# Optimization experiments

Hardware: AMD Instinct MI355X
Metric: run time of the kernel (lower is better)

The kernel has to match this reference:

```python
import jax, jax.numpy as jnp
import numpy as np

D_MODEL = 2048
NUM_HEADS = 32
NUM_GROUPS = 8
HEAD_DIM = D_MODEL // NUM_HEADS  # 64
HEADS_PER_GROUP = NUM_HEADS // NUM_GROUPS  # 4


def setup_inputs() -> dict:
    key = jax.random.key(0)
    ks = jax.random.split(key, 5)
    B, S = 1, 2048
    x = jax.random.normal(ks[0], (B, S, D_MODEL), dtype=jnp.float32)
    scale = 1.0 / np.sqrt(D_MODEL)
    w_q = jax.random.normal(ks[1], (D_MODEL, D_MODEL), dtype=jnp.float32) * scale
    w_k = jax.random.normal(ks[2], (D_MODEL, NUM_GROUPS * HEAD_DIM), dtype=jnp.float32) * scale
    w_v = jax.random.normal(ks[3], (D_MODEL, NUM_GROUPS * HEAD_DIM), dtype=jnp.float32) * scale
    w_o = jax.random.normal(ks[4], (D_MODEL, D_MODEL), dtype=jnp.float32) * scale
    return {"x": x, "w_q": w_q, "w_k": w_k, "w_v": w_v, "w_o": w_o}


def reference(x, w_q, w_k, w_v, w_o):
    B, S, _ = x.shape
    # projections (nn.Linear, no bias)
    q = (x @ w_q).reshape(B, S, NUM_HEADS, HEAD_DIM)          # [B,S,H,d]
    k = (x @ w_k).reshape(B, S, NUM_GROUPS, HEAD_DIM)         # [B,S,G,d]
    v = (x @ w_v).reshape(B, S, NUM_GROUPS, HEAD_DIM)
    # group queries: [B,S,G,hpg,d] so each KV group serves heads_per_group query heads
    qg = q.reshape(B, S, NUM_GROUPS, HEADS_PER_GROUP, HEAD_DIM)
    scale = 1.0 / jnp.sqrt(jnp.asarray(HEAD_DIM, dtype=x.dtype))
    # scores: [B,G,hpg,S_q,S_k] without duplicating K/V
    scores = jnp.einsum("bsghd,btgd->bghst", qg, k) * scale
    attn = jax.nn.softmax(scores, axis=-1)
    out = jnp.einsum("bghst,btgd->bsghd", attn, v)            # [B,S,G,hpg,d]
    out = out.reshape(B, S, D_MODEL)
    return out @ w_o
```

## Files before the change

### kernel.cpp

```cpp
#include <hip/hip_runtime.h>

typedef unsigned short ushort_t;
typedef __attribute__((ext_vector_type(8))) short short8;
typedef __attribute__((ext_vector_type(4))) float floatx4;

__device__ __forceinline__ unsigned short f2bf(float f) {
  unsigned int u = __float_as_uint(f);
  u += 0x7fffu + ((u >> 16) & 1u);
  return (unsigned short)(u >> 16);
}

__device__ __forceinline__ void gl_lds16(const void* g, void* l) {
  __builtin_amdgcn_global_load_lds((const __attribute__((address_space(1))) void*)g,
                                   (__attribute__((address_space(3))) void*)l,
                                   16, 0, 0);
}


__global__ void conv_x_kernel(const float* __restrict__ src, ushort_t* __restrict__ dst, int n4) {
  int i = blockIdx.x * blockDim.x + threadIdx.x;
  if (i >= n4) return;
  float4 v = ((const float4*)src)[i];
  union { ushort_t u[4]; unsigned long long ll; } o;
  o.u[0] = f2bf(v.x); o.u[1] = f2bf(v.y); o.u[2] = f2bf(v.z); o.u[3] = f2bf(v.w);
  ((unsigned long long*)dst)[i] = o.ll;
}

__global__ void transpose_conv(const float* __restrict__ src, ushort_t* __restrict__ dst,
                               int R, int C) {
  __shared__ float tile[32][33];
  int c0 = blockIdx.x * 32, r0 = blockIdx.y * 32;
  int tx = threadIdx.x, ty = threadIdx.y;
#pragma unroll
  for (int i = ty; i < 32; i += 8)
    tile[i][tx] = src[(long)(r0 + i) * C + c0 + tx];
  __syncthreads();
#pragma unroll
  for (int i = ty; i < 32; i += 8)
    dst[(long)(c0 + i) * R + r0 + tx] = f2bf(tile[tx][i]);
}

template <int EPI>
__global__ __launch_bounds__(256, 2) void gemm_bt(
    const ushort_t* __restrict__ A, const ushort_t* __restrict__ B,
    float* __restrict__ C,
    ushort_t* __restrict__ qb, ushort_t* __restrict__ kb, ushort_t* __restrict__ vb,
    int M, int N, int K) {
  __shared__ ushort_t As[128 * 32];
  __shared__ ushort_t Bs[128 * 32];
  const int t = threadIdx.x;
  const int w = t >> 6, lane = t & 63;
  const int m = lane & 15, quad = lane >> 4;
  const int m0 = blockIdx.y * 128, n0 = blockIdx.x * 128;
  const int wr = w >> 1, wc = w & 1;

  floatx4 acc[4][4] = {};

  for (int kk = 0; kk < K; kk += 32) {
    __syncthreads();
#pragma unroll
    for (int i = 0; i < 2; ++i) {
      int c = i * 256 + t;
      int c0 = i * 256 + w * 64;
      gl_lds16(A + (long)(m0 + (c >> 2)) * K + kk + (c & 3) * 8, As + c0 * 8);
      gl_lds16(B + (long)(n0 + (c >> 2)) * K + kk + (c & 3) * 8, Bs + c0 * 8);
    }
    __syncthreads();
    short8 af[4], bf[4];
#pragma unroll
    for (int i = 0; i < 4; ++i)
      af[i] = *(const short8*)(As + (wr * 64 + i * 16 + m) * 32 + quad * 8);
#pragma unroll
    for (int j = 0; j < 4; ++j)
      bf[j] = *(const short8*)(Bs + (wc * 64 + j * 16 + m) * 32 + quad * 8);
#pragma unroll
    for (int i = 0; i < 4; ++i)
#pragma unroll
      for (int j = 0; j < 4; ++j)
        acc[i][j] = __builtin_amdgcn_mfma_f32_16x16x32_bf16(af[i], bf[j], acc[i][j], 0, 0, 0);
  }

#pragma unroll
  for (int i = 0; i < 4; ++i)
#pragma unroll
    for (int j = 0; j < 4; ++j)
#pragma unroll
      for (int r = 0; r < 4; ++r) {
        float v = acc[i][j][r];
        int row = m0 + wr * 64 + i * 16 + quad * 4 + r;
        int col = n0 + wc * 64 + j * 16 + m;
        if (EPI == 1) {
          C[(long)row * N + col] = v;
        } else {
          if (col < 2048) {
            qb[((((col >> 6) * 2048) + row) << 6) | (col & 63)] = f2bf(v * 0.125f);
          } else if (col < 2560) {
            int g = (col - 2048) >> 6;
            kb[(((g * 2048) + row) << 6) | (col & 63)] = f2bf(v);
          } else {
            int g = (col - 2560) >> 6;
            vb[(long)((g << 6) | (col & 63)) * 2048 + row] = f2bf(v);
          }
        }
      }
}

__global__ __launch_bounds__(256, 2) void flash_kernel(
    const ushort_t* __restrict__ Q, const ushort_t* __restrict__ Kb,
    const ushort_t* __restrict__ Vb, ushort_t* __restrict__ O, int S) {
  __shared__ ushort_t Ks[2 * 128 * 32];
  __shared__ ushort_t Vs[4 * 64 * 32];
  __shared__ ushort_t Ps[4 * 4 * 32 * 32];
  const int t = threadIdx.x;
  const int w = t >> 6, lane = t & 63;
  const int m = lane & 15, quad = lane >> 4;
  const int h = blockIdx.y, g = h >> 2;
  const int q0 = blockIdx.x * 128;
  const ushort_t* qp = Q + (long)h * S * 64;
  const ushort_t* kp = Kb + (long)g * S * 64;
  const ushort_t* vp = Vb + (long)g * 64 * S;

  short8 qf[2][2];
#pragma unroll
  for (int rt = 0; rt < 2; ++rt)
#pragma unroll
    for (int kq = 0; kq < 2; ++kq)
      qf[rt][kq] = *(const short8*)(qp + (long)(q0 + w * 32 + rt * 16 + m) * 64 + kq * 32 + quad * 8);

  float mrow[2][4], lrow[2][4];
  floatx4 oacc[2][4] = {};
#pragma unroll
  for (int rt = 0; rt < 2; ++rt)
#pragma unroll
    for (int r = 0; r < 4; ++r) { mrow[rt][r] = -1e30f; lrow[rt][r] = 0.f; }

  ushort_t* Pw = Ps + w * 4096;

  for (int t0 = 0; t0 < S; t0 += 128) {
    __syncthreads();
#pragma unroll
    for (int i = 0; i < 4; ++i) {
      int c = i * 256 + t;
      int c0 = i * 256 + w * 64;
      gl_lds16(kp + (long)(t0 + ((c >> 2) & 127)) * 64 + (c >> 9) * 32 + (c & 3) * 8, Ks + c0 * 8);
      gl_lds16(vp + (long)((c >> 2) & 63) * S + t0 + (c >> 8) * 32 + (c & 3) * 8, Vs + c0 * 8);
    }
    __syncthreads();

    floatx4 sacc[2][8] = {};
#pragma unroll
    for (int ct = 0; ct < 8; ++ct) {
      short8 kf0 = *(const short8*)(Ks + (ct * 16 + m) * 32 + quad * 8);
      short8 kf1 = *(const short8*)(Ks + 4096 + (ct * 16 + m) * 32 + quad * 8);
#pragma unroll
      for (int rt = 0; rt < 2; ++rt) {
        sacc[rt][ct] = __builtin_amdgcn_mfma_f32_16x16x32_bf16(qf[rt][0], kf0, sacc[rt][ct], 0, 0, 0);
        sacc[rt][ct] = __builtin_amdgcn_mfma_f32_16x16x32_bf16(qf[rt][1], kf1, sacc[rt][ct], 0, 0, 0);
      }
    }

    float mnew[2][4], al[2][4], ls[2][4];
#pragma unroll
    for (int rt = 0; rt < 2; ++rt)
#pragma unroll
      for (int r = 0; r < 4; ++r) {
        float mx = sacc[rt][0][r];
#pragma unroll
        for (int ct = 1; ct < 8; ++ct) mx = fmaxf(mx, sacc[rt][ct][r]);
#pragma unroll
        for (int s = 1; s < 16; s <<= 1) mx = fmaxf(mx, __shfl_xor(mx, s));
        mnew[rt][r] = fmaxf(mrow[rt][r], mx);
        al[rt][r] = __expf(mrow[rt][r] - mnew[rt][r]);
        ls[rt][r] = 0.f;
      }

#pragma unroll
    for (int rt = 0; rt < 2; ++rt)
#pragma unroll
      for (int ct = 0; ct < 8; ++ct) {
        int kt = ct >> 1;
        int colbase = (ct & 1) * 16 + m;
#pragma unroll
        for (int r = 0; r < 4; ++r) {
          float p = __expf(sacc[rt][ct][r] - mnew[rt][r]);
          ls[rt][r] += p;
          int row = rt * 16 + quad * 4 + r;
          Pw[kt * 1024 + row * 32 + colbase] = f2bf(p);
        }
      }

#pragma unroll
    for (int rt = 0; rt < 2; ++rt)
#pragma unroll
      for (int r = 0; r < 4; ++r) {
        float s_ = ls[rt][r];
#pragma unroll
        for (int s = 1; s < 16; s <<= 1) s_ += __shfl_xor(s_, s);
        lrow[rt][r] = lrow[rt][r] * al[rt][r] + s_;
        mrow[rt][r] = mnew[rt][r];
      }

#pragma unroll
    for (int rt = 0; rt < 2; ++rt)
#pragma unroll
      for (int ct = 0; ct < 4; ++ct)
#pragma unroll
        for (int r = 0; r < 4; ++r)
          oacc[rt][ct][r] *= al[rt][r];

#pragma unroll
    for (int kt = 0; kt < 4; ++kt) {
      short8 pf[2];
#pragma unroll
      for (int rt = 0; rt < 2; ++rt)
        pf[rt] = *(const short8*)(Pw + kt * 1024 + (rt * 16 + m) * 32 + quad * 8);
#pragma unroll
      for (int ct = 0; ct < 4; ++ct) {
        short8 vf = *(const short8*)(Vs + kt * 2048 + (ct * 16 + m) * 32 + quad * 8);
#pragma unroll
        for (int rt = 0; rt < 2; ++rt)
          oacc[rt][ct] = __builtin_amdgcn_mfma_f32_16x16x32_bf16(pf[rt], vf, oacc[rt][ct], 0, 0, 0);
      }
    }
  }

#pragma unroll
  for (int rt = 0; rt < 2; ++rt)
#pragma unroll
    for (int r = 0; r < 4; ++r) {
      float inv = 1.f / lrow[rt][r];
      int srow = q0 + w * 32 + rt * 16 + quad * 4 + r;
#pragma unroll
      for (int ct = 0; ct < 4; ++ct)
        O[(long)srow * 2048 + h * 64 + ct * 16 + m] = f2bf(oacc[rt][ct][r] * inv);
    }
}


extern "C" void kernel_launch(void* const* d_in, const int* in_sizes, int n_in,
                              void* d_out, int out_size, void* d_ws, size_t ws_size,
                              hipStream_t stream) {
  (void)in_sizes; (void)n_in; (void)out_size; (void)ws_size;
  const float* x  = (const float*)d_in[0];
  const float* wq = (const float*)d_in[1];
  const float* wk = (const float*)d_in[2];
  const float* wv = (const float*)d_in[3];
  const float* wo = (const float*)d_in[4];
  float* out = (float*)d_out;
  char* ws = (char*)d_ws;
  const size_t MB = 1u << 20;

  ushort_t* xb    = (ushort_t*)(ws);
  ushort_t* wqkvT = (ushort_t*)(ws + 8 * MB);
  ushort_t* woT   = (ushort_t*)(ws + 20 * MB);
  ushort_t* qbuf  = (ushort_t*)(ws + 28 * MB);
  ushort_t* kbuf  = (ushort_t*)(ws + 36 * MB);
  ushort_t* vbuf  = (ushort_t*)(ws + 38 * MB);
  ushort_t* attn  = xb;

  conv_x_kernel<<<4096, 256, 0, stream>>>(x, xb, 2048 * 2048 / 4);
  dim3 tb(32, 8);
  transpose_conv<<<dim3(64, 64), tb, 0, stream>>>(wq, wqkvT, 2048, 2048);
  transpose_conv<<<dim3(16, 64), tb, 0, stream>>>(wk, wqkvT + 2048 * 2048, 2048, 512);
  transpose_conv<<<dim3(16, 64), tb, 0, stream>>>(wv, wqkvT + 2560 * 2048, 2048, 512);
  transpose_conv<<<dim3(64, 64), tb, 0, stream>>>(wo, woT, 2048, 2048);

  gemm_bt<0><<<dim3(24, 16), 256, 0, stream>>>(xb, wqkvT, nullptr, qbuf, kbuf, vbuf,
                                               2048, 3072, 2048);
  flash_kernel<<<dim3(16, 32), 256, 0, stream>>>(qbuf, kbuf, vbuf, attn, 2048);
  gemm_bt<1><<<dim3(16, 16), 256, 0, stream>>>(attn, woT, out, nullptr, nullptr, nullptr,
                                               2048, 2048, 2048);
}
```

Before: 289.6 us.

## Keep softmax probabilities in registers via transposed MFMA and shrink GEMM tiles

The flash kernel now computes S^T = K·Q^T so that the softmax probabilities land in registers in the layout the P·V MFMA expects. This removes the per-wave LDS round trip for P, and the row sums are computed with an MFMA against a ones vector instead of shuffles. Exponentials use exp2 with log2(e) folded into the Q scale, and LDS tiles are stored in fragment-ordered layouts so reads are contiguous per lane. The GEMMs switch to 64x128 tiles with more blocks and 3-wave-occupancy launch bounds, trading per-block reuse for more parallelism across the device.

Result: slower. 300.3 us (+3.7%).

```diff
diff --git a/kernel.cpp b/kernel.cpp
--- a/kernel.cpp
+++ b/kernel.cpp
@@ -2,7 +2,18 @@
 
 typedef unsigned short ushort_t;
 typedef __attribute__((ext_vector_type(8))) short short8;
+typedef __attribute__((ext_vector_type(4))) short bf16x4;
 typedef __attribute__((ext_vector_type(4))) float floatx4;
+
+#define MFMA32(A, B, C) __builtin_amdgcn_mfma_f32_16x16x32_bf16(A, B, C, 0, 0, 0)
+
+__device__ __forceinline__ float exp2_(float x) {
+#if __has_builtin(__builtin_amdgcn_exp2f)
+  return __builtin_amdgcn_exp2f(x);
+#else
+  return __builtin_exp2f(x);
+#endif
+}
 
 __device__ __forceinline__ unsigned short f2bf(float f) {
   unsigned int u = __float_as_uint(f);
@@ -15,6 +26,8 @@
                                    (__attribute__((address_space(3))) void*)l,
                                    16, 0, 0);
 }
+
+#define QSCALE 0.18033688011112042f
 
 
 __global__ void conv_x_kernel(const float* __restrict__ src, ushort_t* __restrict__ dst, int n4) {
@@ -41,59 +54,63 @@
 }
 
 template <int EPI>
-__global__ __launch_bounds__(256, 2) void gemm_bt(
+__global__ __launch_bounds__(256, 3) void gemm_bt(
     const ushort_t* __restrict__ A, const ushort_t* __restrict__ B,
     float* __restrict__ C,
     ushort_t* __restrict__ qb, ushort_t* __restrict__ kb, ushort_t* __restrict__ vb,
     int M, int N, int K) {
-  __shared__ ushort_t As[128 * 32];
+  __shared__ ushort_t As[64 * 32];
   __shared__ ushort_t Bs[128 * 32];
   const int t = threadIdx.x;
   const int w = t >> 6, lane = t & 63;
   const int m = lane & 15, quad = lane >> 4;
-  const int m0 = blockIdx.y * 128, n0 = blockIdx.x * 128;
+  const int m0 = blockIdx.y * 64, n0 = blockIdx.x * 128;
   const int wr = w >> 1, wc = w & 1;
 
-  floatx4 acc[4][4] = {};
+  floatx4 acc[2][4] = {};
 
   for (int kk = 0; kk < K; kk += 32) {
     __syncthreads();
+    {
+      int s = t;
+      int m_ = s & 15, qd = (s >> 4) & 3, rt = s >> 6;
+      gl_lds16(A + (long)(m0 + rt * 16 + m_) * K + kk + qd * 8, As + s * 8);
+    }
 #pragma unroll
     for (int i = 0; i < 2; ++i) {
-      int c = i * 256 + t;
-      int c0 = i * 256 + w * 64;
-      gl_lds16(A + (long)(m0 + (c >> 2)) * K + kk + (c & 3) * 8, As + c0 * 8);
-      gl_lds16(B + (long)(n0 + (c >> 2)) * K + kk + (c & 3) * 8, Bs + c0 * 8);
-    }
-    __syncthreads();
-    short8 af[4], bf[4];
-#pragma unroll
-    for (int i = 0; i < 4; ++i)
-      af[i] = *(const short8*)(As + (wr * 64 + i * 16 + m) * 32 + quad * 8);
+      int s = i * 256 + t;
+      int m_ = s & 15, qd = (s >> 4) & 3, ntl = s >> 6;
+      gl_lds16(B + (long)(n0 + ntl * 16 + m_) * K + kk + qd * 8, Bs + s * 8);
+    }
+    __syncthreads();
+    short8 af[2], bf[4];
+#pragma unroll
+    for (int i = 0; i < 2; ++i)
+      af[i] = *(const short8*)(As + ((wr * 2 + i) * 64 + lane) * 8);
 #pragma unroll
     for (int j = 0; j < 4; ++j)
-      bf[j] = *(const short8*)(Bs + (wc * 64 + j * 16 + m) * 32 + quad * 8);
-#pragma unroll
-    for (int i = 0; i < 4; ++i)
+      bf[j] = *(const short8*)(Bs + ((wc * 4 + j) * 64 + lane) * 8);
+#pragma unroll
+    for (int i = 0; i < 2; ++i)
 #pragma unroll
       for (int j = 0; j < 4; ++j)
-        acc[i][j] = __builtin_amdgcn_mfma_f32_16x16x32_bf16(af[i], bf[j], acc[i][j], 0, 0, 0);
+        acc[i][j] = MFMA32(af[i], bf[j], acc[i][j]);
   }
 
 #pragma unroll
-  for (int i = 0; i < 4; ++i)
+  for (int i = 0; i < 2; ++i)
 #pragma unroll
     for (int j = 0; j < 4; ++j)
 #pragma unroll
       for (int r = 0; r < 4; ++r) {
         float v = acc[i][j][r];
-        int row = m0 + wr * 64 + i * 16 + quad * 4 + r;
+        int row = m0 + wr * 32 + i * 16 + quad * 4 + r;
         int col = n0 + wc * 64 + j * 16 + m;
         if (EPI == 1) {
           C[(long)row * N + col] = v;
         } else {
           if (col < 2048) {
-            qb[((((col >> 6) * 2048) + row) << 6) | (col & 63)] = f2bf(v * 0.125f);
+            qb[((((col >> 6) * 2048) + row) << 6) | (col & 63)] = f2bf(v * QSCALE);
           } else if (col < 2560) {
             int g = (col - 2048) >> 6;
             kb[(((g * 2048) + row) << 6) | (col & 63)] = f2bf(v);
@@ -109,131 +126,118 @@
     const ushort_t* __restrict__ Q, const ushort_t* __restrict__ Kb,
     const ushort_t* __restrict__ Vb, ushort_t* __restrict__ O, int S) {
   __shared__ ushort_t Ks[2 * 128 * 32];
-  __shared__ ushort_t Vs[4 * 64 * 32];
-  __shared__ ushort_t Ps[4 * 4 * 32 * 32];
+  __shared__ ushort_t Vs[64 * 128];
   const int t = threadIdx.x;
   const int w = t >> 6, lane = t & 63;
-  const int m = lane & 15, quad = lane >> 4;
+  const int n = lane & 15, quad = lane >> 4;
   const int h = blockIdx.y, g = h >> 2;
-  const int q0 = blockIdx.x * 128;
+  const int q0 = blockIdx.x * 128 + w * 32;
   const ushort_t* qp = Q + (long)h * S * 64;
   const ushort_t* kp = Kb + (long)g * S * 64;
   const ushort_t* vp = Vb + (long)g * 64 * S;
 
   short8 qf[2][2];
 #pragma unroll
-  for (int rt = 0; rt < 2; ++rt)
+  for (int nt = 0; nt < 2; ++nt)
 #pragma unroll
     for (int kq = 0; kq < 2; ++kq)
-      qf[rt][kq] = *(const short8*)(qp + (long)(q0 + w * 32 + rt * 16 + m) * 64 + kq * 32 + quad * 8);
-
-  float mrow[2][4], lrow[2][4];
+      qf[nt][kq] = *(const short8*)(qp + (long)(q0 + nt * 16 + n) * 64 + kq * 32 + quad * 8);
+
+  float mrow[2] = {-3e38f, -3e38f};
+  float lrow[2] = {0.f, 0.f};
   floatx4 oacc[2][4] = {};
-#pragma unroll
-  for (int rt = 0; rt < 2; ++rt)
-#pragma unroll
-    for (int r = 0; r < 4; ++r) { mrow[rt][r] = -1e30f; lrow[rt][r] = 0.f; }
-
-  ushort_t* Pw = Ps + w * 4096;
+  short8 ones8;
+#pragma unroll
+  for (int i = 0; i < 8; ++i) ones8[i] = (short)0x3F80;
 
   for (int t0 = 0; t0 < S; t0 += 128) {
     __syncthreads();
 #pragma unroll
     for (int i = 0; i < 4; ++i) {
-      int c = i * 256 + t;
-      int c0 = i * 256 + w * 64;
-      gl_lds16(kp + (long)(t0 + ((c >> 2) & 127)) * 64 + (c >> 9) * 32 + (c & 3) * 8, Ks + c0 * 8);
-      gl_lds16(vp + (long)((c >> 2) & 63) * S + t0 + (c >> 8) * 32 + (c & 3) * 8, Vs + c0 * 8);
+      int s = i * 256 + t;
+      int m_ = s & 15, qd = (s >> 4) & 3, mt = (s >> 6) & 7, kq = s >> 9;
+      gl_lds16(kp + (long)(t0 + mt * 16 + m_) * 64 + kq * 32 + qd * 8, Ks + s * 8);
+    }
+#pragma unroll
+    for (int i = 0; i < 4; ++i) {
+      int s = i * 256 + t;
+      int m_ = s & 15, ct = (s >> 4) & 3, th = (s >> 6) & 1, mt = s >> 7;
+      gl_lds16(vp + (long)(ct * 16 + m_) * S + t0 + mt * 16 + th * 8, Vs + s * 8);
     }
     __syncthreads();
 
     floatx4 sacc[2][8] = {};
 #pragma unroll
-    for (int ct = 0; ct < 8; ++ct) {
-      short8 kf0 = *(const short8*)(Ks + (ct * 16 + m) * 32 + quad * 8);
-      short8 kf1 = *(const short8*)(Ks + 4096 + (ct * 16 + m) * 32 + quad * 8);
-#pragma unroll
-      for (int rt = 0; rt < 2; ++rt) {
-        sacc[rt][ct] = __builtin_amdgcn_mfma_f32_16x16x32_bf16(qf[rt][0], kf0, sacc[rt][ct], 0, 0, 0);
-        sacc[rt][ct] = __builtin_amdgcn_mfma_f32_16x16x32_bf16(qf[rt][1], kf1, sacc[rt][ct], 0, 0, 0);
-      }
-    }
-
-    float mnew[2][4], al[2][4], ls[2][4];
-#pragma unroll
-    for (int rt = 0; rt < 2; ++rt)
-#pragma unroll
-      for (int r = 0; r < 4; ++r) {
-        float mx = sacc[rt][0][r];
-#pragma unroll
-        for (int ct = 1; ct < 8; ++ct) mx = fmaxf(mx, sacc[rt][ct][r]);
-#pragma unroll
-        for (int s = 1; s < 16; s <<= 1) mx = fmaxf(mx, __shfl_xor(mx, s));
-        mnew[rt][r] = fmaxf(mrow[rt][r], mx);
-        al[rt][r] = __expf(mrow[rt][r] - mnew[rt][r]);
-        ls[rt][r] = 0.f;
-      }
-
-#pragma unroll
-    for (int rt = 0; rt < 2; ++rt)
-#pragma unroll
-      for (int ct = 0; ct < 8; ++ct) {
-        int kt = ct >> 1;
-        int colbase = (ct & 1) * 16 + m;
-#pragma unroll
-        for (int r = 0; r < 4; ++r) {
-          float p = __expf(sacc[rt][ct][r] - mnew[rt][r]);
-          ls[rt][r] += p;
-          int row = rt * 16 + quad * 4 + r;
-          Pw[kt * 1024 + row * 32 + colbase] = f2bf(p);
-        }
-      }
-
-#pragma unroll
-    for (int rt = 0; rt < 2; ++rt)
-#pragma unroll
-      for (int r = 0; r < 4; ++r) {
-        float s_ = ls[rt][r];
-#pragma unroll
-        for (int s = 1; s < 16; s <<= 1) s_ += __shfl_xor(s_, s);
-        lrow[rt][r] = lrow[rt][r] * al[rt][r] + s_;
-        mrow[rt][r] = mnew[rt][r];
-      }
-
-#pragma unroll
-    for (int rt = 0; rt < 2; ++rt)
+    for (int mt = 0; mt < 8; ++mt) {
+      short8 a0 = *(const short8*)(Ks + (mt * 64 + lane) * 8);
+      short8 a1 = *(const short8*)(Ks + ((8 + mt) * 64 + lane) * 8);
+#pragma unroll
+      for (int nt = 0; nt < 2; ++nt) {
+        sacc[nt][mt] = MFMA32(a0, qf[nt][0], sacc[nt][mt]);
+        sacc[nt][mt] = MFMA32(a1, qf[nt][1], sacc[nt][mt]);
+      }
+    }
+
+    short8 P8[2][4];
+#pragma unroll
+    for (int nt = 0; nt < 2; ++nt) {
+      float mx = -3e38f;
+#pragma unroll
+      for (int mt = 0; mt < 8; ++mt)
+#pragma unroll
+        for (int r = 0; r < 4; ++r) mx = fmaxf(mx, sacc[nt][mt][r]);
+      mx = fmaxf(mx, __shfl_xor(mx, 16));
+      mx = fmaxf(mx, __shfl_xor(mx, 32));
+      float mnew = fmaxf(mrow[nt], mx);
+      float alpha = exp2_(mrow[nt] - mnew);
+      mrow[nt] = mnew;
+#pragma unroll
+      for (int mt = 0; mt < 8; ++mt) {
+        int p = mt >> 1, hh = (mt & 1) * 4;
+#pragma unroll
+        for (int r = 0; r < 4; ++r)
+          P8[nt][p][hh + r] = (short)f2bf(exp2_(sacc[nt][mt][r] - mnew));
+      }
+      floatx4 lacc = {};
+#pragma unroll
+      for (int p = 0; p < 4; ++p)
+        lacc = MFMA32(ones8, P8[nt][p], lacc);
+      lrow[nt] = lrow[nt] * alpha + lacc[0];
 #pragma unroll
       for (int ct = 0; ct < 4; ++ct)
 #pragma unroll
-        for (int r = 0; r < 4; ++r)
-          oacc[rt][ct][r] *= al[rt][r];
-
-#pragma unroll
-    for (int kt = 0; kt < 4; ++kt) {
-      short8 pf[2];
-#pragma unroll
-      for (int rt = 0; rt < 2; ++rt)
-        pf[rt] = *(const short8*)(Pw + kt * 1024 + (rt * 16 + m) * 32 + quad * 8);
+        for (int r = 0; r < 4; ++r) oacc[nt][ct][r] *= alpha;
+    }
+
+#pragma unroll
+    for (int p = 0; p < 4; ++p) {
+      short8 vf[4];
 #pragma unroll
       for (int ct = 0; ct < 4; ++ct) {
-        short8 vf = *(const short8*)(Vs + kt * 2048 + (ct * 16 + m) * 32 + quad * 8);
-#pragma unroll
-        for (int rt = 0; rt < 2; ++rt)
-          oacc[rt][ct] = __builtin_amdgcn_mfma_f32_16x16x32_bf16(pf[rt], vf, oacc[rt][ct], 0, 0, 0);
-      }
+        bf16x4 lo = *(const bf16x4*)(Vs + (((2 * p) * 2 + (quad >> 1)) * 4 + ct) * 128 + n * 8 + (quad & 1) * 4);
+        bf16x4 hi = *(const bf16x4*)(Vs + (((2 * p + 1) * 2 + (quad >> 1)) * 4 + ct) * 128 + n * 8 + (quad & 1) * 4);
+        vf[ct] = __builtin_shufflevector(lo, hi, 0, 1, 2, 3, 4, 5, 6, 7);
+      }
+#pragma unroll
+      for (int nt = 0; nt < 2; ++nt)
+#pragma unroll
+        for (int ct = 0; ct < 4; ++ct)
+          oacc[nt][ct] = MFMA32(vf[ct], P8[nt][p], oacc[nt][ct]);
     }
   }
 
 #pragma unroll
-  for (int rt = 0; rt < 2; ++rt)
-#pragma unroll
-    for (int r = 0; r < 4; ++r) {
-      float inv = 1.f / lrow[rt][r];
-      int srow = q0 + w * 32 + rt * 16 + quad * 4 + r;
-#pragma unroll
-      for (int ct = 0; ct < 4; ++ct)
-        O[(long)srow * 2048 + h * 64 + ct * 16 + m] = f2bf(oacc[rt][ct][r] * inv);
-    }
+  for (int nt = 0; nt < 2; ++nt) {
+    float inv = 1.f / lrow[nt];
+    int q = q0 + nt * 16 + n;
+#pragma unroll
+    for (int ct = 0; ct < 4; ++ct) {
+      bf16x4 o4;
+#pragma unroll
+      for (int r = 0; r < 4; ++r) o4[r] = (short)f2bf(oacc[nt][ct][r] * inv);
+      *(bf16x4*)(O + (long)q * 2048 + h * 64 + ct * 16 + quad * 4) = o4;
+    }
+  }
 }
 
 
@@ -265,9 +269,9 @@
   transpose_conv<<<dim3(16, 64), tb, 0, stream>>>(wv, wqkvT + 2560 * 2048, 2048, 512);
   transpose_conv<<<dim3(64, 64), tb, 0, stream>>>(wo, woT, 2048, 2048);
 
-  gemm_bt<0><<<dim3(24, 16), 256, 0, stream>>>(xb, wqkvT, nullptr, qbuf, kbuf, vbuf,
+  gemm_bt<0><<<dim3(24, 32), 256, 0, stream>>>(xb, wqkvT, nullptr, qbuf, kbuf, vbuf,
                                                2048, 3072, 2048);
   flash_kernel<<<dim3(16, 32), 256, 0, stream>>>(qbuf, kbuf, vbuf, attn, 2048);
-  gemm_bt<1><<<dim3(16, 16), 256, 0, stream>>>(attn, woT, out, nullptr, nullptr, nullptr,
+  gemm_bt<1><<<dim3(16, 32), 256, 0, stream>>>(attn, woT, out, nullptr, nullptr, nullptr,
                                                2048, 2048, 2048);
 }
```
